# Kernel tuning notes

Measured on AMD Instinct MI355X. Metric: run time of the kernel, lower is better.

The kernel has to match this reference:

```python
import jax, jax.numpy as jnp
import numpy as np

DIM = 192
HEADS = 6
HSP = 8
WSP = 8
POS_DIM = (DIM // 4) // 4  # 12


def _ln(x, g, b, eps=1e-5):
    m = jnp.mean(x, -1, keepdims=True)
    v = jnp.mean((x - m) ** 2, -1, keepdims=True)
    return (x - m) / jnp.sqrt(v + eps) * g + b


def _rel_tables():
    # rpe_biases: ((2*HSP-1)*(2*WSP-1), 2) float coords of all relative offsets
    bh, bw = np.meshgrid(np.arange(1 - HSP, HSP), np.arange(1 - WSP, WSP), indexing='ij')
    biases = np.stack([bh, bw], -1).reshape(-1, 2).astype(np.float32)
    # relative_position_index: (N, N) int lookup into the bias table
    ch, cw = np.meshgrid(np.arange(HSP), np.arange(WSP), indexing='ij')
    coords = np.stack([ch, cw], 0).reshape(2, -1)  # (2, N)
    rel = coords[:, :, None] - coords[:, None, :]  # (2, N, N)
    idx = (rel[0] + HSP - 1) * (2 * WSP - 1) + (rel[1] + WSP - 1)
    return jnp.asarray(biases), jnp.asarray(idx.astype(np.int32))


def setup_inputs() -> dict:
    key = jax.random.key(0)
    ks = jax.random.split(key, 8)
    B, H, W = 2, 256, 256
    L = H * W
    def lin(k, i, o):
        return jax.random.normal(k, (i, o), jnp.float32) * 0.02
    return {
        'qkv': jax.random.normal(ks[0], (3, B, L, DIM), jnp.float32),
        'w_proj': lin(ks[1], 2, POS_DIM), 'b_proj': jnp.zeros((POS_DIM,), jnp.float32),
        'g1': jnp.ones((POS_DIM,), jnp.float32), 'be1': jnp.zeros((POS_DIM,), jnp.float32),
        'w1': lin(ks[2], POS_DIM, POS_DIM), 'b1': jnp.zeros((POS_DIM,), jnp.float32),
        'g2': jnp.ones((POS_DIM,), jnp.float32), 'be2': jnp.zeros((POS_DIM,), jnp.float32),
        'w2': lin(ks[3], POS_DIM, POS_DIM), 'b2': jnp.zeros((POS_DIM,), jnp.float32),
        'g3': jnp.ones((POS_DIM,), jnp.float32), 'be3': jnp.zeros((POS_DIM,), jnp.float32),
        'w3': lin(ks[4], POS_DIM, HEADS), 'b3': jnp.zeros((HEADS,), jnp.float32),
        'H': H, 'W': W,
    }


def reference(qkv, w_proj, b_proj, g1, be1, w1, b1, g2, be2, w2, b2, g3, be3, w3, b3, H, W):
    B, L, C = qkv.shape[1], qkv.shape[2], qkv.shape[3]
    hd = C // HEADS
    scale = float(hd) ** -0.5
    N = HSP * WSP

    def im2win(x):
        # (B, L, C) -> (B*nW, heads, N, hd)
        x = x.reshape(B, H // HSP, HSP, W // WSP, WSP, C)
        x = x.transpose(0, 1, 3, 2, 4, 5).reshape(-1, N, HEADS, hd)
        return x.transpose(0, 2, 1, 3)

    q = im2win(qkv[0]) * scale
    k = im2win(qkv[1])
    v = im2win(qkv[2])

    attn = jnp.einsum('whnd,whmd->whnm', q, k)  # (B*nW, heads, N, N)

    # dynamic relative position bias via MLP (DynamicPosBias, residual=False)
    biases, rel_idx = _rel_tables()
    p = biases @ w_proj + b_proj
    p = jax.nn.relu(_ln(p, g1, be1)) @ w1 + b1
    p = jax.nn.relu(_ln(p, g2, be2)) @ w2 + b2
    p = jax.nn.relu(_ln(p, g3, be3)) @ w3 + b3  # (n_rel, heads)
    rpb = p[rel_idx.reshape(-1)].reshape(N, N, HEADS).transpose(2, 0, 1)  # (heads, N, N)
    attn = attn + rpb[None]

    attn = jax.nn.softmax(attn, axis=-1)
    x = jnp.einsum('whnm,whmd->whnd', attn, v)  # (B*nW, heads, N, hd)
    x = x.transpose(0, 2, 1, 3).reshape(-1, N, C)

    # windows2img: (B*nW, N, C) -> (B, H, W, C)
    x = x.reshape(B, H // HSP, W // WSP, HSP, WSP, C)
    x = x.transpose(0, 1, 3, 2, 4, 5).reshape(B, H, W, C)
    return x
```

## Files before the change

kernel.cpp:

```cpp
#include <hip/hip_runtime.h>

#define NHEADS 6
#define HD 32
#define CDIM 192
#define NTOK 64
#define NREL 225
#define PDIM 12
#define IMG 256
#define NWW 32
#define NWIN 2048
#define SCALE 0.17677669529663687f

typedef __attribute__((ext_vector_type(8))) short v8s;
typedef __attribute__((ext_vector_type(4))) float v4f;

#define QKS 40
#define VTS 72
#define ATS 68
#define PTS 72

__device__ __forceinline__ unsigned short f2bf(float f) {
    union { float f; unsigned u; } c; c.f = f;
    unsigned u = c.u + 0x7fffu + ((c.u >> 16) & 1u);
    return (unsigned short)(u >> 16);
}

__device__ __forceinline__ void ln_relu12(const float* x, const float* g,
                                          const float* be, float* y) {
    float m = 0.f;
#pragma unroll
    for (int i = 0; i < PDIM; ++i) m += x[i];
    m *= (1.f / PDIM);
    float v = 0.f;
#pragma unroll
    for (int i = 0; i < PDIM; ++i) { float d = x[i] - m; v += d * d; }
    v *= (1.f / PDIM);
    float inv = rsqrtf(v + 1e-5f);
#pragma unroll
    for (int i = 0; i < PDIM; ++i) {
        float t = (x[i] - m) * inv * g[i] + be[i];
        y[i] = t > 0.f ? t : 0.f;
    }
}

__global__ __launch_bounds__(256) void posbias_kernel(
    const float* __restrict__ wp, const float* __restrict__ bp,
    const float* __restrict__ g1, const float* __restrict__ be1,
    const float* __restrict__ w1, const float* __restrict__ b1,
    const float* __restrict__ g2, const float* __restrict__ be2,
    const float* __restrict__ w2, const float* __restrict__ b2,
    const float* __restrict__ g3, const float* __restrict__ be3,
    const float* __restrict__ w3, const float* __restrict__ b3,
    float* __restrict__ rpb)
{
    __shared__ float p_sh[NREL * NHEADS];
    int r = threadIdx.x;
    if (r < NREL) {
        float x0 = (float)(r / 15 - 7);
        float x1 = (float)(r % 15 - 7);
        float h[PDIM], y[PDIM];
#pragma unroll
        for (int o = 0; o < PDIM; ++o)
            h[o] = x0 * wp[o] + x1 * wp[PDIM + o] + bp[o];
        ln_relu12(h, g1, be1, y);
#pragma unroll
        for (int o = 0; o < PDIM; ++o) {
            float a = b1[o];
#pragma unroll
            for (int i = 0; i < PDIM; ++i) a += y[i] * w1[i * PDIM + o];
            h[o] = a;
        }
        ln_relu12(h, g2, be2, y);
#pragma unroll
        for (int o = 0; o < PDIM; ++o) {
            float a = b2[o];
#pragma unroll
            for (int i = 0; i < PDIM; ++i) a += y[i] * w2[i * PDIM + o];
            h[o] = a;
        }
        ln_relu12(h, g3, be3, y);
#pragma unroll
        for (int o = 0; o < NHEADS; ++o) {
            float a = b3[o];
#pragma unroll
            for (int i = 0; i < PDIM; ++i) a += y[i] * w3[i * NHEADS + o];
            p_sh[r * NHEADS + o] = a;
        }
    }
    __syncthreads();
    for (int i = threadIdx.x; i < NHEADS * NTOK * NTOK; i += 256) {
        int h = i >> 12;
        int n = (i >> 6) & 63;
        int m = i & 63;
        int idx = ((n >> 3) - (m >> 3) + 7) * 15 + ((n & 7) - (m & 7) + 7);
        rpb[i] = p_sh[idx * NHEADS + h];
    }
}

__global__ __launch_bounds__(256) void win_attn_mfma(
    const float* __restrict__ qkv, const float* __restrict__ rpb,
    float* __restrict__ out)
{
    __shared__ unsigned short qs[NTOK * QKS];
    __shared__ unsigned short ks[NTOK * QKS];
    __shared__ unsigned short vt[HD * VTS];
    __shared__ float at[NTOK * ATS];
    unsigned short* pt = (unsigned short*)at;

    const int t = threadIdx.x;
    const int head = blockIdx.x >> 11;
    const int win  = blockIdx.x & (NWIN - 1);
    const int b    = win >> 10;
    const int bh   = (win >> 5) & 31;
    const int bw   = win & 31;

    const size_t SST = (size_t)2 * IMG * IMG * CDIM;
    const float* basep = qkv + (size_t)b * IMG * IMG * CDIM;
#pragma unroll
    for (int pass = 0; pass < 2; ++pass) {
        int idx = t + pass * 256;
        int tok = idx >> 3;
        int d   = (idx & 7) * 4;
        size_t loff = ((size_t)(bh * 8 + (tok >> 3)) * IMG + (bw * 8 + (tok & 7))) * CDIM
                    + head * HD + d;
        float4 q4 = *(const float4*)(basep + loff);
        float4 k4 = *(const float4*)(basep + SST + loff);
        float4 v4 = *(const float4*)(basep + 2 * SST + loff);
        *(ushort4*)&qs[tok * QKS + d] = make_ushort4(
            f2bf(q4.x * SCALE), f2bf(q4.y * SCALE), f2bf(q4.z * SCALE), f2bf(q4.w * SCALE));
        *(ushort4*)&ks[tok * QKS + d] = make_ushort4(
            f2bf(k4.x), f2bf(k4.y), f2bf(k4.z), f2bf(k4.w));
        vt[(d + 0) * VTS + tok] = f2bf(v4.x);
        vt[(d + 1) * VTS + tok] = f2bf(v4.y);
        vt[(d + 2) * VTS + tok] = f2bf(v4.z);
        vt[(d + 3) * VTS + tok] = f2bf(v4.w);
    }
    __syncthreads();

    const int wave = t >> 6;
    const int lane = t & 63;
    const int lw = lane & 15;
    const int lg = lane >> 4;
    const int rowbase = wave * 16;

    {
        const float* rpbh = rpb + head * NTOK * NTOK;
        v8s a = *(const v8s*)&qs[(rowbase + lw) * QKS + lg * 8];
        v4f acc[4];
#pragma unroll
        for (int ct = 0; ct < 4; ++ct) {
#pragma unroll
            for (int r = 0; r < 4; ++r)
                acc[ct][r] = rpbh[(rowbase + lg * 4 + r) * NTOK + ct * 16 + lw];
            v8s bfr = *(const v8s*)&ks[(ct * 16 + lw) * QKS + lg * 8];
            acc[ct] = __builtin_amdgcn_mfma_f32_16x16x32_bf16(a, bfr, acc[ct], 0, 0, 0);
        }
#pragma unroll
        for (int ct = 0; ct < 4; ++ct)
#pragma unroll
            for (int r = 0; r < 4; ++r)
                at[(rowbase + lg * 4 + r) * ATS + ct * 16 + lw] = acc[ct][r];
    }
    __syncthreads();

    {
        const int r  = t >> 2;
        const int cb = (t & 3) * 16;
        float x[16];
#pragma unroll
        for (int kk = 0; kk < 4; ++kk) {
            float4 x4 = *(const float4*)&at[r * ATS + cb + 4 * kk];
            x[4 * kk + 0] = x4.x; x[4 * kk + 1] = x4.y;
            x[4 * kk + 2] = x4.z; x[4 * kk + 3] = x4.w;
        }
        float mx = x[0];
#pragma unroll
        for (int i = 1; i < 16; ++i) mx = fmaxf(mx, x[i]);
        mx = fmaxf(mx, __shfl_xor(mx, 1));
        mx = fmaxf(mx, __shfl_xor(mx, 2));
        float s = 0.f;
#pragma unroll
        for (int i = 0; i < 16; ++i) { x[i] = __expf(x[i] - mx); s += x[i]; }
        s += __shfl_xor(s, 1);
        s += __shfl_xor(s, 2);
        float rinv = 1.f / s;
        v8s pw0, pw1;
#pragma unroll
        for (int i = 0; i < 8; ++i) pw0[i] = (short)f2bf(x[i] * rinv);
#pragma unroll
        for (int i = 0; i < 8; ++i) pw1[i] = (short)f2bf(x[8 + i] * rinv);
        __syncthreads();
        *(v8s*)&pt[r * PTS + cb]     = pw0;
        *(v8s*)&pt[r * PTS + cb + 8] = pw1;
    }
    __syncthreads();

    {
        v8s pa[2];
#pragma unroll
        for (int kt = 0; kt < 2; ++kt)
            pa[kt] = *(const v8s*)&pt[(rowbase + lw) * PTS + kt * 32 + lg * 8];
        v4f acc2[2] = {};
#pragma unroll
        for (int dt = 0; dt < 2; ++dt)
#pragma unroll
            for (int kt = 0; kt < 2; ++kt) {
                v8s vb = *(const v8s*)&vt[(dt * 16 + lw) * VTS + kt * 32 + lg * 8];
                acc2[dt] = __builtin_amdgcn_mfma_f32_16x16x32_bf16(pa[kt], vb, acc2[dt], 0, 0, 0);
            }
#pragma unroll
        for (int dt = 0; dt < 2; ++dt)
#pragma unroll
            for (int r = 0; r < 4; ++r) {
                int n = rowbase + lg * 4 + r;
                size_t off = (((size_t)b * IMG + bh * 8 + (n >> 3)) * IMG
                              + (bw * 8 + (n & 7))) * CDIM + head * HD + dt * 16 + lw;
                out[off] = acc2[dt][r];
            }
    }
}

extern "C" void kernel_launch(void* const* d_in, const int* in_sizes, int n_in,
                              void* d_out, int out_size, void* d_ws, size_t ws_size,
                              hipStream_t stream) {
    const float* qkv = (const float*)d_in[0];
    const float* wp  = (const float*)d_in[1];
    const float* bp  = (const float*)d_in[2];
    const float* g1  = (const float*)d_in[3];
    const float* be1 = (const float*)d_in[4];
    const float* w1  = (const float*)d_in[5];
    const float* b1  = (const float*)d_in[6];
    const float* g2  = (const float*)d_in[7];
    const float* be2 = (const float*)d_in[8];
    const float* w2  = (const float*)d_in[9];
    const float* b2  = (const float*)d_in[10];
    const float* g3  = (const float*)d_in[11];
    const float* be3 = (const float*)d_in[12];
    const float* w3  = (const float*)d_in[13];
    const float* b3  = (const float*)d_in[14];

    float* rpb = (float*)d_ws;
    posbias_kernel<<<1, 256, 0, stream>>>(wp, bp, g1, be1, w1, b1,
                                          g2, be2, w2, b2, g3, be3, w3, b3, rpb);
    win_attn_mfma<<<NWIN * NHEADS, 256, 0, stream>>>(qkv, rpb, (float*)d_out);
}
```

Measured before the change: 101.0 us.

## Do softmax in MFMA registers, prefetch bias, and parallelize posbias across blocks

The attention kernel now runs the softmax directly on the MFMA accumulator registers, using cross-lane shuffles within each 16-lane group. This drops the fp32 score staging buffer in shared memory and two barriers, which lowers LDS use and may let more blocks run per CU. The relative-position bias is loaded into registers before the QKV loads so its latency overlaps with them. The posbias kernel now launches 96 blocks, each recomputing the small MLP and writing one slice of the bias table, instead of a single block looping over the whole table.

Result: faster. 96.75 us (-4.2%).

```diff
diff --git a/kernel.cpp b/kernel.cpp
--- a/kernel.cpp
+++ b/kernel.cpp
@@ -16,7 +16,6 @@
 
 #define QKS 40
 #define VTS 72
-#define ATS 68
 #define PTS 72
 
 __device__ __forceinline__ unsigned short f2bf(float f) {
@@ -88,13 +87,12 @@
         }
     }
     __syncthreads();
-    for (int i = threadIdx.x; i < NHEADS * NTOK * NTOK; i += 256) {
-        int h = i >> 12;
-        int n = (i >> 6) & 63;
-        int m = i & 63;
-        int idx = ((n >> 3) - (m >> 3) + 7) * 15 + ((n & 7) - (m & 7) + 7);
-        rpb[i] = p_sh[idx * NHEADS + h];
-    }
+    int i = blockIdx.x * 256 + threadIdx.x;
+    int h = i >> 12;
+    int n = (i >> 6) & 63;
+    int m = i & 63;
+    int idx = ((n >> 3) - (m >> 3) + 7) * 15 + ((n & 7) - (m & 7) + 7);
+    rpb[i] = p_sh[idx * NHEADS + h];
 }
 
 __global__ __launch_bounds__(256) void win_attn_mfma(
@@ -104,8 +102,7 @@
     __shared__ unsigned short qs[NTOK * QKS];
     __shared__ unsigned short ks[NTOK * QKS];
     __shared__ unsigned short vt[HD * VTS];
-    __shared__ float at[NTOK * ATS];
-    unsigned short* pt = (unsigned short*)at;
+    __shared__ unsigned short pt[NTOK * PTS];
 
     const int t = threadIdx.x;
     const int head = blockIdx.x >> 11;
@@ -113,6 +110,22 @@
     const int b    = win >> 10;
     const int bh   = (win >> 5) & 31;
     const int bw   = win & 31;
+
+    const int wave = t >> 6;
+    const int lane = t & 63;
+    const int lw = lane & 15;
+    const int lg = lane >> 4;
+    const int rowbase = wave * 16;
+
+    float rbias[4][4];
+    {
+        const float* rpbh = rpb + head * NTOK * NTOK;
+#pragma unroll
+        for (int ct = 0; ct < 4; ++ct)
+#pragma unroll
+            for (int r = 0; r < 4; ++r)
+                rbias[ct][r] = rpbh[(rowbase + lg * 4 + r) * NTOK + ct * 16 + lw];
+    }
 
     const size_t SST = (size_t)2 * IMG * IMG * CDIM;
     const float* basep = qkv + (size_t)b * IMG * IMG * CDIM;
@@ -137,61 +150,47 @@
     }
     __syncthreads();
 
-    const int wave = t >> 6;
-    const int lane = t & 63;
-    const int lw = lane & 15;
-    const int lg = lane >> 4;
-    const int rowbase = wave * 16;
-
     {
-        const float* rpbh = rpb + head * NTOK * NTOK;
         v8s a = *(const v8s*)&qs[(rowbase + lw) * QKS + lg * 8];
         v4f acc[4];
 #pragma unroll
         for (int ct = 0; ct < 4; ++ct) {
 #pragma unroll
-            for (int r = 0; r < 4; ++r)
-                acc[ct][r] = rpbh[(rowbase + lg * 4 + r) * NTOK + ct * 16 + lw];
+            for (int r = 0; r < 4; ++r) acc[ct][r] = rbias[ct][r];
             v8s bfr = *(const v8s*)&ks[(ct * 16 + lw) * QKS + lg * 8];
             acc[ct] = __builtin_amdgcn_mfma_f32_16x16x32_bf16(a, bfr, acc[ct], 0, 0, 0);
         }
+        v4f mx4;
+#pragma unroll
+        for (int r = 0; r < 4; ++r)
+            mx4[r] = fmaxf(fmaxf(acc[0][r], acc[1][r]), fmaxf(acc[2][r], acc[3][r]));
+#pragma unroll
+        for (int off = 1; off < 16; off <<= 1)
+#pragma unroll
+            for (int r = 0; r < 4; ++r)
+                mx4[r] = fmaxf(mx4[r], __shfl_xor(mx4[r], off));
+        v4f s4 = {0.f, 0.f, 0.f, 0.f};
 #pragma unroll
         for (int ct = 0; ct < 4; ++ct)
 #pragma unroll
-            for (int r = 0; r < 4; ++r)
-                at[(rowbase + lg * 4 + r) * ATS + ct * 16 + lw] = acc[ct][r];
-    }
-    __syncthreads();
-
-    {
-        const int r  = t >> 2;
-        const int cb = (t & 3) * 16;
-        float x[16];
-#pragma unroll
-        for (int kk = 0; kk < 4; ++kk) {
-            float4 x4 = *(const float4*)&at[r * ATS + cb + 4 * kk];
-            x[4 * kk + 0] = x4.x; x[4 * kk + 1] = x4.y;
-            x[4 * kk + 2] = x4.z; x[4 * kk + 3] = x4.w;
-        }
-        float mx = x[0];
-#pragma unroll
-        for (int i = 1; i < 16; ++i) mx = fmaxf(mx, x[i]);
-        mx = fmaxf(mx, __shfl_xor(mx, 1));
-        mx = fmaxf(mx, __shfl_xor(mx, 2));
-        float s = 0.f;
-#pragma unroll
-        for (int i = 0; i < 16; ++i) { x[i] = __expf(x[i] - mx); s += x[i]; }
-        s += __shfl_xor(s, 1);
-        s += __shfl_xor(s, 2);
-        float rinv = 1.f / s;
-        v8s pw0, pw1;
-#pragma unroll
-        for (int i = 0; i < 8; ++i) pw0[i] = (short)f2bf(x[i] * rinv);
-#pragma unroll
-        for (int i = 0; i < 8; ++i) pw1[i] = (short)f2bf(x[8 + i] * rinv);
-        __syncthreads();
-        *(v8s*)&pt[r * PTS + cb]     = pw0;
-        *(v8s*)&pt[r * PTS + cb + 8] = pw1;
+            for (int r = 0; r < 4; ++r) {
+                acc[ct][r] = __expf(acc[ct][r] - mx4[r]);
+                s4[r] += acc[ct][r];
+            }
+#pragma unroll
+        for (int off = 1; off < 16; off <<= 1)
+#pragma unroll
+            for (int r = 0; r < 4; ++r)
+                s4[r] += __shfl_xor(s4[r], off);
+        v4f rinv;
+#pragma unroll
+        for (int r = 0; r < 4; ++r) rinv[r] = 1.f / s4[r];
+#pragma unroll
+        for (int ct = 0; ct < 4; ++ct)
+#pragma unroll
+            for (int r = 0; r < 4; ++r)
+                pt[(rowbase + lg * 4 + r) * PTS + ct * 16 + lw] =
+                    f2bf(acc[ct][r] * rinv[r]);
     }
     __syncthreads();
 
@@ -240,7 +239,7 @@
     const float* b3  = (const float*)d_in[14];
 
     float* rpb = (float*)d_ws;
-    posbias_kernel<<<1, 256, 0, stream>>>(wp, bp, g1, be1, w1, b1,
-                                          g2, be2, w2, b2, g3, be3, w3, b3, rpb);
+    posbias_kernel<<<96, 256, 0, stream>>>(wp, bp, g1, be1, w1, b1,
+                                           g2, be2, w2, b2, g3, be3, w3, b3, rpb);
     win_attn_mfma<<<NWIN * NHEADS, 256, 0, stream>>>(qkv, rpb, (float*)d_out);
 }
```
